# Kernel optimization log

Hardware: AMD Instinct MI355X
Metric: run time of the kernel (lower is better)

Reference implementation:

```python
import jax, jax.numpy as jnp
import numpy as np

IN_CAPS, IN_SIZE = 1152, 8
OUT_CAPS, OUT_SIZE = 10, 16
ROUTING_ITERS = 3
BATCH = 512


def squash(s, axis=-1):
    # v = ||s||^2 / (1 + ||s||^2) * s / ||s||
    sq = jnp.sum(s * s, axis=axis, keepdims=True)
    return s * (sq / (1.0 + sq)) / jnp.sqrt(sq + 1e-8)


def setup_inputs() -> dict:
    key = jax.random.key(0)
    k1, k2 = jax.random.split(key)
    x = jax.random.normal(k1, (BATCH, IN_CAPS, IN_SIZE), dtype=jnp.float32)
    W = jax.random.normal(k2, (IN_CAPS, OUT_CAPS, OUT_SIZE, IN_SIZE), dtype=jnp.float32)
    return {"x": x, "W": W}


def reference(x, W):
    # u_hat[b,i,o,:] = W[i,o] @ x[b,i]  -> (B, 1152, 10, 16)
    u_hat = jnp.einsum('iops,bis->biop', W, x)
    u_det = jax.lax.stop_gradient(u_hat)
    # routing logits, shared across batch: (1152, 10)
    b_ij = jnp.zeros((IN_CAPS, OUT_CAPS), dtype=x.dtype)
    v = None
    for it in range(ROUTING_ITERS):
        # legacy F.softmax on 4D (1,I,O,1) defaults to dim=1 -> over in_capsules
        c_ij = jax.nn.softmax(b_ij, axis=0)  # (I, O)
        if it == ROUTING_ITERS - 1:
            s_j = jnp.einsum('io,biop->bop', c_ij, u_hat)  # (B, 10, 16)
            v = squash(s_j, axis=-1)
        else:
            s_j = jnp.einsum('io,biop->bop', c_ij, u_det)
            v = squash(s_j, axis=-1)
            # agreement: mean over batch of u_hat . v -> (I, O)
            agree = jnp.mean(jnp.einsum('biop,bop->bio', u_det, v), axis=0)
            b_ij = b_ij + agree
    return v  # (B, 10, 16)
```

## Files before the change

### kernel.cpp

```cpp
#include <hip/hip_runtime.h>


#define IC 1152
#define OC 10
#define PS 16
#define SS 8
#define NB 512
#define KD (IC * SS)
#define ND (OC * PS)

#define G1_BM 128
#define G1_NSPLIT 128
#define G1_KSP (KD / G1_NSPLIT)
#define G1_KC 36

#define G2_BCH 32
#define G2_NBS (NB / G2_BCH)
#define G2_NKT (KD / 64)

__global__ void prep_wr(const float* __restrict__ W, float* __restrict__ wr)
{
    const int q = blockIdx.x * 256 + threadIdx.x;
    const int k = q / 40;
    const int n4 = q - k * 40;
    const int i = k >> 3, s = k & 7;
    const int o = n4 >> 2;
    const int p0 = (n4 << 2) & 15;
    const float* wsrc = W + (((size_t)(i * OC + o) * PS) + p0) * SS + s;
    float4 t;
    t.x = wsrc[0]; t.y = wsrc[SS]; t.z = wsrc[2 * SS]; t.w = wsrc[3 * SS];
    *(float4*)(wr + (size_t)q * 4) = t;
}

__global__ void softmax_col(const float* __restrict__ bij, float* __restrict__ c)
{
    const int o = blockIdx.x;
    const int tid = threadIdx.x;
    __shared__ float red[256];

    float m = -3.4e38f;
    for (int i = tid; i < IC; i += 256) m = fmaxf(m, bij[i * OC + o]);
    red[tid] = m;
    __syncthreads();
    for (int st = 128; st > 0; st >>= 1) {
        if (tid < st) red[tid] = fmaxf(red[tid], red[tid + st]);
        __syncthreads();
    }
    m = red[0];
    __syncthreads();

    float sum = 0.f;
    for (int i = tid; i < IC; i += 256) sum += expf(bij[i * OC + o] - m);
    red[tid] = sum;
    __syncthreads();
    for (int st = 128; st > 0; st >>= 1) {
        if (tid < st) red[tid] += red[tid + st];
        __syncthreads();
    }
    const float inv = 1.0f / red[0];

    for (int i = tid; i < IC; i += 256)
        c[i * OC + o] = expf(bij[i * OC + o] - m) * inv;
}

__global__ __launch_bounds__(256, 2) void gemm1_fused(const float* __restrict__ x,
                                                      const float* __restrict__ wr,
                                                      const float* __restrict__ c,
                                                      float* __restrict__ part)
{
    __shared__ __align__(16) float xl[G1_KC][G1_BM + 4];
    __shared__ __align__(16) float wl[G1_KC][ND + 4];
    __shared__ float cl[96];

    const int tid = threadIdx.x;
    const int mb = blockIdx.x & 3;
    const int ks = blockIdx.x >> 2;
    const int m0 = mb * G1_BM;
    const int k0s = ks * G1_KSP;
    const int cg = tid & 15, rg = tid >> 4;
    const int c0 = cg * 10, r0 = rg * 8;

    if (tid < 90) cl[tid] = c ? c[ks * 90 + tid] : (1.0f / 1152.0f);
    __syncthreads();

    float acc[8][10] = {};

    for (int kc = 0; kc < G1_KSP; kc += G1_KC) {
        const int k0 = k0s + kc;
        for (int q = tid; q < (G1_BM * G1_KC / 4); q += 256) {
            const int r = q / 9, kv4 = q - r * 9;
            const float4 t = *(const float4*)(x + (size_t)(m0 + r) * KD + k0 + kv4 * 4);
            xl[kv4 * 4 + 0][r] = t.x;
            xl[kv4 * 4 + 1][r] = t.y;
            xl[kv4 * 4 + 2][r] = t.z;
            xl[kv4 * 4 + 3][r] = t.w;
        }
        for (int q = tid; q < (G1_KC * 40); q += 256) {
            const int rr = q / 40, c4 = q - rr * 40;
            float4 t = *(const float4*)(wr + (size_t)(k0 + rr) * ND + c4 * 4);
            const float sc = cl[(((kc + rr) >> 3) * 10) + (c4 >> 2)];
            t.x *= sc; t.y *= sc; t.z *= sc; t.w *= sc;
            *(float4*)&wl[rr][c4 * 4] = t;
        }
        __syncthreads();
#pragma unroll 4
        for (int kk = 0; kk < G1_KC; ++kk) {
            const float4 a0 = *(const float4*)&xl[kk][r0];
            const float4 a1 = *(const float4*)&xl[kk][r0 + 4];
            const float2 w0 = *(const float2*)&wl[kk][c0 + 0];
            const float2 w1 = *(const float2*)&wl[kk][c0 + 2];
            const float2 w2 = *(const float2*)&wl[kk][c0 + 4];
            const float2 w3 = *(const float2*)&wl[kk][c0 + 6];
            const float2 w4 = *(const float2*)&wl[kk][c0 + 8];
            const float av[8] = { a0.x, a0.y, a0.z, a0.w, a1.x, a1.y, a1.z, a1.w };
            const float wv[10] = { w0.x, w0.y, w1.x, w1.y, w2.x,
                                   w2.y, w3.x, w3.y, w4.x, w4.y };
#pragma unroll
            for (int r = 0; r < 8; ++r)
#pragma unroll
                for (int n = 0; n < 10; ++n)
                    acc[r][n] += av[r] * wv[n];
        }
        __syncthreads();
    }

    float* dst = part + (size_t)ks * (NB * ND);
#pragma unroll
    for (int r = 0; r < 8; ++r) {
        float* row = dst + (size_t)(m0 + r0 + r) * ND + c0;
#pragma unroll
        for (int n = 0; n < 5; ++n)
            *(float2*)(row + n * 2) = *(const float2*)&acc[r][n * 2];
    }
}

__global__ void reduce_squash(const float* __restrict__ part, float* __restrict__ out)
{
    const int t = blockIdx.x * 128 + threadIdx.x;
    const int idx = t >> 2, q = t & 3;
    const float* src = part + (size_t)idx * 16 + q * 4;
    float4 a = { 0, 0, 0, 0 };
#pragma unroll 8
    for (int sp = 0; sp < G1_NSPLIT; ++sp) {
        const float4 p = *(const float4*)(src + (size_t)sp * (NB * ND));
        a.x += p.x; a.y += p.y; a.z += p.z; a.w += p.w;
    }
    float sq = a.x * a.x + a.y * a.y + a.z * a.z + a.w * a.w;
    sq += __shfl_xor(sq, 1);
    sq += __shfl_xor(sq, 2);
    const float f = (sq / (1.0f + sq)) / sqrtf(sq + 1e-8f);
    a.x *= f; a.y *= f; a.z *= f; a.w *= f;
    *(float4*)(out + (size_t)idx * 16 + q * 4) = a;
}

__global__ __launch_bounds__(128, 2) void gemm2_agree(const float* __restrict__ x,
                                                      const float* __restrict__ v,
                                                      const float* __restrict__ wr,
                                                      float* __restrict__ bij)
{
    __shared__ __align__(16) float xl[G2_BCH][68];
    __shared__ __align__(16) float vl[G2_BCH][164];
    __shared__ float agr[80];

    const int tid = threadIdx.x;
    const int kt = blockIdx.x % G2_NKT;
    const int bs = blockIdx.x / G2_NKT;
    const int k0 = kt * 64, b0 = bs * G2_BCH;
    const int cg = tid & 15, rg = tid >> 4;
    const int c0 = cg * 10, r0 = rg * 8;

    if (tid < 80) agr[tid] = 0.f;

    for (int q = tid; q < G2_BCH * 16; q += 128) {
        const int bb = q >> 4, kv = q & 15;
        *(float4*)&xl[bb][kv * 4] = *(const float4*)(x + (size_t)(b0 + bb) * KD + k0 + kv * 4);
    }
    for (int q = tid; q < G2_BCH * 40; q += 128) {
        const int bb = q / 40, nv = q - bb * 40;
        *(float4*)&vl[bb][nv * 4] = *(const float4*)(v + (size_t)(b0 + bb) * ND + nv * 4);
    }
    __syncthreads();

    float acc[8][10] = {};
#pragma unroll 4
    for (int bb = 0; bb < G2_BCH; ++bb) {
        const float4 a0 = *(const float4*)&xl[bb][r0];
        const float4 a1 = *(const float4*)&xl[bb][r0 + 4];
        const float2 w0 = *(const float2*)&vl[bb][c0 + 0];
        const float2 w1 = *(const float2*)&vl[bb][c0 + 2];
        const float2 w2 = *(const float2*)&vl[bb][c0 + 4];
        const float2 w3 = *(const float2*)&vl[bb][c0 + 6];
        const float2 w4 = *(const float2*)&vl[bb][c0 + 8];
        const float av[8] = { a0.x, a0.y, a0.z, a0.w, a1.x, a1.y, a1.z, a1.w };
        const float wv[10] = { w0.x, w0.y, w1.x, w1.y, w2.x,
                               w2.y, w3.x, w3.y, w4.x, w4.y };
#pragma unroll
        for (int r = 0; r < 8; ++r)
#pragma unroll
            for (int n = 0; n < 10; ++n)
                acc[r][n] += av[r] * wv[n];
    }

    const int o0 = c0 >> 4;
    const int nsp = (o0 + 1) * 16 - c0;
    float sum0 = 0.f, sum1 = 0.f;
#pragma unroll
    for (int r = 0; r < 8; ++r) {
        const float* wrow = wr + (size_t)(k0 + r0 + r) * ND + c0;
#pragma unroll
        for (int n = 0; n < 10; ++n) {
            const float t = acc[r][n] * wrow[n];
            if (n < nsp) sum0 += t; else sum1 += t;
        }
    }
    atomicAdd(&agr[rg * 10 + o0], sum0);
    if (nsp < 10) atomicAdd(&agr[rg * 10 + o0 + 1], sum1);
    __syncthreads();

    if (tid < 80) atomicAdd(bij + kt * 80 + tid, agr[tid] * (1.0f / 512.0f));
}

extern "C" void kernel_launch(void* const* d_in, const int* in_sizes, int n_in,
                              void* d_out, int out_size, void* d_ws, size_t ws_size,
                              hipStream_t stream)
{
    (void)in_sizes; (void)n_in; (void)out_size; (void)ws_size;
    const float* x = (const float*)d_in[0];
    const float* W = (const float*)d_in[1];
    float* out = (float*)d_out;
    float* ws = (float*)d_ws;

    float* b_ij = ws;
    float* cbuf = ws + 11520;
    float* wrb  = ws + 23040;
    float* part = ws + 1497600;
    float* vbuf = ws + 11983360;

    hipMemsetAsync(b_ij, 0, IC * OC * sizeof(float), stream);
    prep_wr<<<1440, 256, 0, stream>>>(W, wrb);

    for (int it = 0; it < 3; ++it) {
        const float* cptr = nullptr;
        if (it > 0) {
            softmax_col<<<OC, 256, 0, stream>>>(b_ij, cbuf);
            cptr = cbuf;
        }
        gemm1_fused<<<G1_NSPLIT * 4, 256, 0, stream>>>(x, wrb, cptr, part);
        reduce_squash<<<160, 128, 0, stream>>>(part, (it == 2) ? out : vbuf);
        if (it < 2)
            gemm2_agree<<<G2_NKT * G2_NBS, 128, 0, stream>>>(x, vbuf, wrb, b_ij);
    }
}
```

Before: 263.9 us.

## Fuse all routing stages into one persistent kernel with grid barriers

Replaces the sequence of separate launches (weight reorder, softmax, split-K GEMM, reduce+squash, agreement GEMM) with a single persistent kernel of 512 blocks that uses atomic-counter grid barriers between stages. The softmax over b_ij is now recomputed redundantly in every block instead of in a separate tiny kernel, and the reduce and agreement stages are retiled to use all 512 blocks. The aim is to remove kernel launch gaps and tail effects across about a dozen launches. The trade-offs are that correctness depends on all 512 blocks being co-resident, and that the barriers add spin-wait overhead.

```diff
diff --git a/kernel.cpp b/kernel.cpp
--- a/kernel.cpp
+++ b/kernel.cpp
@@ -6,218 +6,270 @@
 #define PS 16
 #define SS 8
 #define NB 512
-#define KD (IC * SS)
-#define ND (OC * PS)
-
-#define G1_BM 128
-#define G1_NSPLIT 128
-#define G1_KSP (KD / G1_NSPLIT)
-#define G1_KC 36
-
-#define G2_BCH 32
-#define G2_NBS (NB / G2_BCH)
-#define G2_NKT (KD / 64)
-
-__global__ void prep_wr(const float* __restrict__ W, float* __restrict__ wr)
+#define KD 9216
+#define ND 160
+
+#define GRID 512
+#define BLK 256
+
+#define P1_BM 128
+#define P1_KSP 72
+#define P1_KC 36
+
+#define P3_KT 96
+#define P3_NKT 96
+#define P3_BCH 32
+
+__device__ __forceinline__ void gbar(unsigned* slot)
 {
-    const int q = blockIdx.x * 256 + threadIdx.x;
-    const int k = q / 40;
-    const int n4 = q - k * 40;
-    const int i = k >> 3, s = k & 7;
-    const int o = n4 >> 2;
-    const int p0 = (n4 << 2) & 15;
-    const float* wsrc = W + (((size_t)(i * OC + o) * PS) + p0) * SS + s;
-    float4 t;
-    t.x = wsrc[0]; t.y = wsrc[SS]; t.z = wsrc[2 * SS]; t.w = wsrc[3 * SS];
-    *(float4*)(wr + (size_t)q * 4) = t;
-}
-
-__global__ void softmax_col(const float* __restrict__ bij, float* __restrict__ c)
-{
-    const int o = blockIdx.x;
-    const int tid = threadIdx.x;
-    __shared__ float red[256];
-
-    float m = -3.4e38f;
-    for (int i = tid; i < IC; i += 256) m = fmaxf(m, bij[i * OC + o]);
-    red[tid] = m;
     __syncthreads();
-    for (int st = 128; st > 0; st >>= 1) {
-        if (tid < st) red[tid] = fmaxf(red[tid], red[tid + st]);
-        __syncthreads();
-    }
-    m = red[0];
-    __syncthreads();
-
-    float sum = 0.f;
-    for (int i = tid; i < IC; i += 256) sum += expf(bij[i * OC + o] - m);
-    red[tid] = sum;
-    __syncthreads();
-    for (int st = 128; st > 0; st >>= 1) {
-        if (tid < st) red[tid] += red[tid + st];
-        __syncthreads();
-    }
-    const float inv = 1.0f / red[0];
-
-    for (int i = tid; i < IC; i += 256)
-        c[i * OC + o] = expf(bij[i * OC + o] - m) * inv;
-}
-
-__global__ __launch_bounds__(256, 2) void gemm1_fused(const float* __restrict__ x,
-                                                      const float* __restrict__ wr,
-                                                      const float* __restrict__ c,
-                                                      float* __restrict__ part)
-{
-    __shared__ __align__(16) float xl[G1_KC][G1_BM + 4];
-    __shared__ __align__(16) float wl[G1_KC][ND + 4];
-    __shared__ float cl[96];
-
-    const int tid = threadIdx.x;
-    const int mb = blockIdx.x & 3;
-    const int ks = blockIdx.x >> 2;
-    const int m0 = mb * G1_BM;
-    const int k0s = ks * G1_KSP;
-    const int cg = tid & 15, rg = tid >> 4;
-    const int c0 = cg * 10, r0 = rg * 8;
-
-    if (tid < 90) cl[tid] = c ? c[ks * 90 + tid] : (1.0f / 1152.0f);
-    __syncthreads();
-
-    float acc[8][10] = {};
-
-    for (int kc = 0; kc < G1_KSP; kc += G1_KC) {
-        const int k0 = k0s + kc;
-        for (int q = tid; q < (G1_BM * G1_KC / 4); q += 256) {
-            const int r = q / 9, kv4 = q - r * 9;
-            const float4 t = *(const float4*)(x + (size_t)(m0 + r) * KD + k0 + kv4 * 4);
-            xl[kv4 * 4 + 0][r] = t.x;
-            xl[kv4 * 4 + 1][r] = t.y;
-            xl[kv4 * 4 + 2][r] = t.z;
-            xl[kv4 * 4 + 3][r] = t.w;
-        }
-        for (int q = tid; q < (G1_KC * 40); q += 256) {
-            const int rr = q / 40, c4 = q - rr * 40;
-            float4 t = *(const float4*)(wr + (size_t)(k0 + rr) * ND + c4 * 4);
-            const float sc = cl[(((kc + rr) >> 3) * 10) + (c4 >> 2)];
-            t.x *= sc; t.y *= sc; t.z *= sc; t.w *= sc;
-            *(float4*)&wl[rr][c4 * 4] = t;
-        }
-        __syncthreads();
-#pragma unroll 4
-        for (int kk = 0; kk < G1_KC; ++kk) {
-            const float4 a0 = *(const float4*)&xl[kk][r0];
-            const float4 a1 = *(const float4*)&xl[kk][r0 + 4];
-            const float2 w0 = *(const float2*)&wl[kk][c0 + 0];
-            const float2 w1 = *(const float2*)&wl[kk][c0 + 2];
-            const float2 w2 = *(const float2*)&wl[kk][c0 + 4];
-            const float2 w3 = *(const float2*)&wl[kk][c0 + 6];
-            const float2 w4 = *(const float2*)&wl[kk][c0 + 8];
-            const float av[8] = { a0.x, a0.y, a0.z, a0.w, a1.x, a1.y, a1.z, a1.w };
-            const float wv[10] = { w0.x, w0.y, w1.x, w1.y, w2.x,
-                                   w2.y, w3.x, w3.y, w4.x, w4.y };
-#pragma unroll
-            for (int r = 0; r < 8; ++r)
-#pragma unroll
-                for (int n = 0; n < 10; ++n)
-                    acc[r][n] += av[r] * wv[n];
-        }
-        __syncthreads();
-    }
-
-    float* dst = part + (size_t)ks * (NB * ND);
-#pragma unroll
-    for (int r = 0; r < 8; ++r) {
-        float* row = dst + (size_t)(m0 + r0 + r) * ND + c0;
-#pragma unroll
-        for (int n = 0; n < 5; ++n)
-            *(float2*)(row + n * 2) = *(const float2*)&acc[r][n * 2];
-    }
-}
-
-__global__ void reduce_squash(const float* __restrict__ part, float* __restrict__ out)
-{
-    const int t = blockIdx.x * 128 + threadIdx.x;
-    const int idx = t >> 2, q = t & 3;
-    const float* src = part + (size_t)idx * 16 + q * 4;
-    float4 a = { 0, 0, 0, 0 };
-#pragma unroll 8
-    for (int sp = 0; sp < G1_NSPLIT; ++sp) {
-        const float4 p = *(const float4*)(src + (size_t)sp * (NB * ND));
-        a.x += p.x; a.y += p.y; a.z += p.z; a.w += p.w;
-    }
-    float sq = a.x * a.x + a.y * a.y + a.z * a.z + a.w * a.w;
-    sq += __shfl_xor(sq, 1);
-    sq += __shfl_xor(sq, 2);
-    const float f = (sq / (1.0f + sq)) / sqrtf(sq + 1e-8f);
-    a.x *= f; a.y *= f; a.z *= f; a.w *= f;
-    *(float4*)(out + (size_t)idx * 16 + q * 4) = a;
-}
-
-__global__ __launch_bounds__(128, 2) void gemm2_agree(const float* __restrict__ x,
-                                                      const float* __restrict__ v,
-                                                      const float* __restrict__ wr,
-                                                      float* __restrict__ bij)
-{
-    __shared__ __align__(16) float xl[G2_BCH][68];
-    __shared__ __align__(16) float vl[G2_BCH][164];
-    __shared__ float agr[80];
-
-    const int tid = threadIdx.x;
-    const int kt = blockIdx.x % G2_NKT;
-    const int bs = blockIdx.x / G2_NKT;
-    const int k0 = kt * 64, b0 = bs * G2_BCH;
-    const int cg = tid & 15, rg = tid >> 4;
-    const int c0 = cg * 10, r0 = rg * 8;
-
-    if (tid < 80) agr[tid] = 0.f;
-
-    for (int q = tid; q < G2_BCH * 16; q += 128) {
-        const int bb = q >> 4, kv = q & 15;
-        *(float4*)&xl[bb][kv * 4] = *(const float4*)(x + (size_t)(b0 + bb) * KD + k0 + kv * 4);
-    }
-    for (int q = tid; q < G2_BCH * 40; q += 128) {
-        const int bb = q / 40, nv = q - bb * 40;
-        *(float4*)&vl[bb][nv * 4] = *(const float4*)(v + (size_t)(b0 + bb) * ND + nv * 4);
+    if (threadIdx.x == 0) {
+        __threadfence();
+        __hip_atomic_fetch_add(slot, 1u, __ATOMIC_RELEASE, __HIP_MEMORY_SCOPE_AGENT);
+        while (__hip_atomic_load(slot, __ATOMIC_ACQUIRE, __HIP_MEMORY_SCOPE_AGENT) < (unsigned)GRID)
+            __builtin_amdgcn_s_sleep(1);
+        __threadfence();
     }
     __syncthreads();
-
-    float acc[8][10] = {};
+}
+
+__global__ __launch_bounds__(BLK, 2) void digitcaps_mega(const float* __restrict__ x,
+                                                         const float* __restrict__ W,
+                                                         float* __restrict__ out,
+                                                         float* __restrict__ ws)
+{
+    __shared__ __align__(16) char smem[43008];
+    __shared__ float agr[120];
+    __shared__ float sm[344];
+
+    float* b_ij = ws;
+    float* wrb  = ws + 11520;
+    float* part = ws + 1486080;
+    float* vbuf = ws + 11971840;
+    unsigned* bar = (unsigned*)(ws + 12053760);
+
+    const int tid = threadIdx.x;
+    const int bid = blockIdx.x;
+    const int gid = bid * BLK + tid;
+    const int cgx = tid & 15, rgx = tid >> 4;
+    const int c0 = cgx * 10;
+
+    float (*xl1)[132] = (float (*)[132])smem;
+    float (*wl1)[164] = (float (*)[164])(smem + 19008);
+    float* cl         = (float*)(smem + 42624);
+    float (*xl3)[100] = (float (*)[100])smem;
+    float (*vl3)[164] = (float (*)[164])(smem + 12800);
+
+    int slot = 0;
+
+    if (gid < IC * OC) b_ij[gid] = 0.f;
+    for (int q = gid; q < (KD * ND) / 4; q += GRID * BLK) {
+        const int k = q / 40;
+        const int n4 = q - k * 40;
+        const int i = k >> 3, s = k & 7;
+        const int o = n4 >> 2;
+        const int p0 = (n4 << 2) & 15;
+        const float* wsrc = W + (((size_t)(i * OC + o) * PS) + p0) * SS + s;
+        float4 t;
+        t.x = wsrc[0]; t.y = wsrc[SS]; t.z = wsrc[2 * SS]; t.w = wsrc[3 * SS];
+        *(float4*)(wrb + (size_t)q * 4) = t;
+    }
+    gbar(&bar[slot++]);
+
+    for (int it = 0; it < 3; ++it) {
+        {
+            const int mb = bid & 3, ks = bid >> 2;
+            const int m0 = mb * P1_BM, k0s = ks * P1_KSP;
+            const int r0 = rgx * 8;
+
+            if (it == 0) {
+                if (tid < 90) cl[tid] = 1.0f / 1152.0f;
+            } else {
+                if (tid < 160) {
+                    const int o = tid % 10, seg = tid / 10;
+                    const float* bp = b_ij + o;
+                    float m = -3.4e38f;
+                    for (int i = seg * 72; i < seg * 72 + 72; ++i)
+                        m = fmaxf(m, bp[i * 10]);
+                    sm[o * 16 + seg] = m;
+                }
+                __syncthreads();
+                if (tid < 10) {
+                    float m = sm[tid * 16];
+                    for (int s2 = 1; s2 < 16; ++s2) m = fmaxf(m, sm[tid * 16 + s2]);
+                    sm[320 + tid] = m;
+                }
+                __syncthreads();
+                if (tid < 160) {
+                    const int o = tid % 10, seg = tid / 10;
+                    const float mo = sm[320 + o];
+                    const float* bp = b_ij + o;
+                    float s = 0.f;
+                    for (int i = seg * 72; i < seg * 72 + 72; ++i)
+                        s += expf(bp[i * 10] - mo);
+                    sm[160 + o * 16 + seg] = s;
+                }
+                __syncthreads();
+                if (tid < 10) {
+                    float s = 0.f;
+                    for (int s2 = 0; s2 < 16; ++s2) s += sm[160 + tid * 16 + s2];
+                    sm[330 + tid] = 1.0f / s;
+                }
+                __syncthreads();
+                if (tid < 90) {
+                    const int il = tid / 10, o = tid % 10;
+                    const int i = ks * 9 + il;
+                    cl[tid] = expf(b_ij[i * 10 + o] - sm[320 + o]) * sm[330 + o];
+                }
+            }
+            __syncthreads();
+
+            float acc[8][10] = {};
+            for (int kc = 0; kc < P1_KSP; kc += P1_KC) {
+                const int k0 = k0s + kc;
+                for (int q = tid; q < 1152; q += BLK) {
+                    const int r = q / 9, kv4 = q - r * 9;
+                    const float4 t = *(const float4*)(x + (size_t)(m0 + r) * KD + k0 + kv4 * 4);
+                    xl1[kv4 * 4 + 0][r] = t.x;
+                    xl1[kv4 * 4 + 1][r] = t.y;
+                    xl1[kv4 * 4 + 2][r] = t.z;
+                    xl1[kv4 * 4 + 3][r] = t.w;
+                }
+                for (int q = tid; q < 1440; q += BLK) {
+                    const int rr = q / 40, c4 = q - rr * 40;
+                    float4 t = *(const float4*)(wrb + (size_t)(k0 + rr) * ND + c4 * 4);
+                    const float sc = cl[(((kc + rr) >> 3) * 10) + (c4 >> 2)];
+                    t.x *= sc; t.y *= sc; t.z *= sc; t.w *= sc;
+                    *(float4*)&wl1[rr][c4 * 4] = t;
+                }
+                __syncthreads();
 #pragma unroll 4
-    for (int bb = 0; bb < G2_BCH; ++bb) {
-        const float4 a0 = *(const float4*)&xl[bb][r0];
-        const float4 a1 = *(const float4*)&xl[bb][r0 + 4];
-        const float2 w0 = *(const float2*)&vl[bb][c0 + 0];
-        const float2 w1 = *(const float2*)&vl[bb][c0 + 2];
-        const float2 w2 = *(const float2*)&vl[bb][c0 + 4];
-        const float2 w3 = *(const float2*)&vl[bb][c0 + 6];
-        const float2 w4 = *(const float2*)&vl[bb][c0 + 8];
-        const float av[8] = { a0.x, a0.y, a0.z, a0.w, a1.x, a1.y, a1.z, a1.w };
-        const float wv[10] = { w0.x, w0.y, w1.x, w1.y, w2.x,
-                               w2.y, w3.x, w3.y, w4.x, w4.y };
-#pragma unroll
-        for (int r = 0; r < 8; ++r)
-#pragma unroll
-            for (int n = 0; n < 10; ++n)
-                acc[r][n] += av[r] * wv[n];
-    }
-
-    const int o0 = c0 >> 4;
-    const int nsp = (o0 + 1) * 16 - c0;
-    float sum0 = 0.f, sum1 = 0.f;
-#pragma unroll
-    for (int r = 0; r < 8; ++r) {
-        const float* wrow = wr + (size_t)(k0 + r0 + r) * ND + c0;
-#pragma unroll
-        for (int n = 0; n < 10; ++n) {
-            const float t = acc[r][n] * wrow[n];
-            if (n < nsp) sum0 += t; else sum1 += t;
+                for (int kk = 0; kk < P1_KC; ++kk) {
+                    const float4 a0 = *(const float4*)&xl1[kk][r0];
+                    const float4 a1 = *(const float4*)&xl1[kk][r0 + 4];
+                    const float2 w0 = *(const float2*)&wl1[kk][c0 + 0];
+                    const float2 w1 = *(const float2*)&wl1[kk][c0 + 2];
+                    const float2 w2 = *(const float2*)&wl1[kk][c0 + 4];
+                    const float2 w3 = *(const float2*)&wl1[kk][c0 + 6];
+                    const float2 w4 = *(const float2*)&wl1[kk][c0 + 8];
+                    const float av[8] = { a0.x, a0.y, a0.z, a0.w, a1.x, a1.y, a1.z, a1.w };
+                    const float wv[10] = { w0.x, w0.y, w1.x, w1.y, w2.x,
+                                           w2.y, w3.x, w3.y, w4.x, w4.y };
+#pragma unroll
+                    for (int r = 0; r < 8; ++r)
+#pragma unroll
+                        for (int n = 0; n < 10; ++n)
+                            acc[r][n] += av[r] * wv[n];
+                }
+                __syncthreads();
+            }
+            float* dst = part + (size_t)ks * (NB * ND);
+#pragma unroll
+            for (int r = 0; r < 8; ++r) {
+                float* row = dst + (size_t)(m0 + r0 + r) * ND + c0;
+#pragma unroll
+                for (int n = 0; n < 5; ++n)
+                    *(float2*)(row + n * 2) = *(const float2*)&acc[r][n * 2];
+            }
+        }
+        gbar(&bar[slot++]);
+
+        {
+            float* dst = (it == 2) ? out : vbuf;
+            if (gid < 81920) {
+                const int bo = gid >> 4;
+                const int sub = gid & 15;
+                const int h = sub >> 2, q = sub & 3;
+                const float* src = part + (size_t)bo * 16 + q * 4;
+                float4 a = { 0, 0, 0, 0 };
+#pragma unroll 8
+                for (int j = 0; j < 32; ++j) {
+                    const float4 p = *(const float4*)(src + (size_t)(h + 4 * j) * (NB * ND));
+                    a.x += p.x; a.y += p.y; a.z += p.z; a.w += p.w;
+                }
+                a.x += __shfl_xor(a.x, 4); a.y += __shfl_xor(a.y, 4);
+                a.z += __shfl_xor(a.z, 4); a.w += __shfl_xor(a.w, 4);
+                a.x += __shfl_xor(a.x, 8); a.y += __shfl_xor(a.y, 8);
+                a.z += __shfl_xor(a.z, 8); a.w += __shfl_xor(a.w, 8);
+                float sq = a.x * a.x + a.y * a.y + a.z * a.z + a.w * a.w;
+                sq += __shfl_xor(sq, 1);
+                sq += __shfl_xor(sq, 2);
+                const float f = (sq / (1.0f + sq)) / sqrtf(sq + 1e-8f);
+                if (h == 0) {
+                    float4 r;
+                    r.x = a.x * f; r.y = a.y * f; r.z = a.z * f; r.w = a.w * f;
+                    *(float4*)(dst + (size_t)bo * 16 + q * 4) = r;
+                }
+            }
+        }
+
+        if (it < 2) {
+            gbar(&bar[slot++]);
+            {
+                const int r0 = rgx * 6;
+                const int o0 = c0 >> 4;
+                const int nsp = (o0 + 1) * 16 - c0;
+                for (int rep = 0; rep < 3; ++rep) {
+                    const int vt = bid * 3 + rep;
+                    const int kt = vt % P3_NKT;
+                    const int bs = vt / P3_NKT;
+                    const int k0 = kt * P3_KT, b0 = bs * P3_BCH;
+                    if (tid < 120) agr[tid] = 0.f;
+                    for (int q = tid; q < 768; q += BLK) {
+                        const int bb = q / 24, kv = q - bb * 24;
+                        *(float4*)&xl3[bb][kv * 4] =
+                            *(const float4*)(x + (size_t)(b0 + bb) * KD + k0 + kv * 4);
+                    }
+                    for (int q = tid; q < 1280; q += BLK) {
+                        const int bb = q / 40, nv = q - bb * 40;
+                        *(float4*)&vl3[bb][nv * 4] =
+                            *(const float4*)(vbuf + (size_t)(b0 + bb) * ND + nv * 4);
+                    }
+                    __syncthreads();
+
+                    float acc[6][10] = {};
+#pragma unroll 4
+                    for (int bb = 0; bb < P3_BCH; ++bb) {
+                        const float2 x0 = *(const float2*)&xl3[bb][r0];
+                        const float2 x1 = *(const float2*)&xl3[bb][r0 + 2];
+                        const float2 x2 = *(const float2*)&xl3[bb][r0 + 4];
+                        const float2 w0 = *(const float2*)&vl3[bb][c0 + 0];
+                        const float2 w1 = *(const float2*)&vl3[bb][c0 + 2];
+                        const float2 w2 = *(const float2*)&vl3[bb][c0 + 4];
+                        const float2 w3 = *(const float2*)&vl3[bb][c0 + 6];
+                        const float2 w4 = *(const float2*)&vl3[bb][c0 + 8];
+                        const float av[6] = { x0.x, x0.y, x1.x, x1.y, x2.x, x2.y };
+                        const float wv[10] = { w0.x, w0.y, w1.x, w1.y, w2.x,
+                                               w2.y, w3.x, w3.y, w4.x, w4.y };
+#pragma unroll
+                        for (int r = 0; r < 6; ++r)
+#pragma unroll
+                            for (int n = 0; n < 10; ++n)
+                                acc[r][n] += av[r] * wv[n];
+                    }
+
+#pragma unroll
+                    for (int r = 0; r < 6; ++r) {
+                        const int row = r0 + r;
+                        const int il = row >> 3;
+                        const float* wrow = wrb + (size_t)(k0 + row) * ND + c0;
+                        float s0 = 0.f, s1 = 0.f;
+#pragma unroll
+                        for (int n = 0; n < 10; ++n) {
+                            const float t = acc[r][n] * wrow[n];
+                            if (n < nsp) s0 += t; else s1 += t;
+                        }
+                        atomicAdd(&agr[il * 10 + o0], s0);
+                        if (nsp < 10) atomicAdd(&agr[il * 10 + o0 + 1], s1);
+                    }
+                    __syncthreads();
+                    if (tid < 120) atomicAdd(&b_ij[kt * 120 + tid], agr[tid] * (1.0f / 512.0f));
+                    __syncthreads();
+                }
+            }
+            gbar(&bar[slot++]);
         }
     }
-    atomicAdd(&agr[rg * 10 + o0], sum0);
-    if (nsp < 10) atomicAdd(&agr[rg * 10 + o0 + 1], sum1);
-    __syncthreads();
-
-    if (tid < 80) atomicAdd(bij + kt * 80 + tid, agr[tid] * (1.0f / 512.0f));
 }
 
 extern "C" void kernel_launch(void* const* d_in, const int* in_sizes, int n_in,
@@ -230,24 +282,6 @@
     float* out = (float*)d_out;
     float* ws = (float*)d_ws;
 
-    float* b_ij = ws;
-    float* cbuf = ws + 11520;
-    float* wrb  = ws + 23040;
-    float* part = ws + 1497600;
-    float* vbuf = ws + 11983360;
-
-    hipMemsetAsync(b_ij, 0, IC * OC * sizeof(float), stream);
-    prep_wr<<<1440, 256, 0, stream>>>(W, wrb);
-
-    for (int it = 0; it < 3; ++it) {
-        const float* cptr = nullptr;
-        if (it > 0) {
-            softmax_col<<<OC, 256, 0, stream>>>(b_ij, cbuf);
-            cptr = cbuf;
-        }
-        gemm1_fused<<<G1_NSPLIT * 4, 256, 0, stream>>>(x, wrb, cptr, part);
-        reduce_squash<<<160, 128, 0, stream>>>(part, (it == 2) ? out : vbuf);
-        if (it < 2)
-            gemm2_agree<<<G2_NKT * G2_NBS, 128, 0, stream>>>(x, vbuf, wrb, b_ij);
-    }
+    hipMemsetAsync(ws + 12053760, 0, 16 * sizeof(unsigned), stream);
+    digitcaps_mega<<<GRID, BLK, 0, stream>>>(x, W, out, ws);
 }
```

Result: slower. 956.7 us (+262.6%).

## Fuse softmax into gemm1, fold memset into prep, widen reduce parallelism

Applied to the files above, without the earlier changes.

Removes the separate softmax_col kernel: every gemm1 block now recomputes the per-column max and sum over all b_ij and derives its own coupling coefficients. The memset of b_ij moves into prep_wr. reduce_squash now spreads the 128-way split reduction over four lanes per output vector and combines them with shuffles, which raises parallelism. Together these remove three launches, but each of the 512 gemm1 blocks repeats the full 11520-element softmax scan in its prologue.

```diff
diff --git a/kernel.cpp b/kernel.cpp
--- a/kernel.cpp
+++ b/kernel.cpp
@@ -6,21 +6,23 @@
 #define PS 16
 #define SS 8
 #define NB 512
-#define KD (IC * SS)
-#define ND (OC * PS)
-
+#define KD 9216
+#define ND 160
+
+#define G1_NS 128
 #define G1_BM 128
-#define G1_NSPLIT 128
-#define G1_KSP (KD / G1_NSPLIT)
+#define G1_KSP 72
 #define G1_KC 36
 
 #define G2_BCH 32
-#define G2_NBS (NB / G2_BCH)
-#define G2_NKT (KD / 64)
-
-__global__ void prep_wr(const float* __restrict__ W, float* __restrict__ wr)
+#define G2_NBS 16
+#define G2_NKT 144
+
+__global__ void prep_wr(const float* __restrict__ W, float* __restrict__ wr,
+                        float* __restrict__ bij)
 {
     const int q = blockIdx.x * 256 + threadIdx.x;
+    if (q < IC * OC) bij[q] = 0.f;
     const int k = q / 40;
     const int n4 = q - k * 40;
     const int i = k >> 3, s = k & 7;
@@ -32,45 +34,16 @@
     *(float4*)(wr + (size_t)q * 4) = t;
 }
 
-__global__ void softmax_col(const float* __restrict__ bij, float* __restrict__ c)
-{
-    const int o = blockIdx.x;
-    const int tid = threadIdx.x;
-    __shared__ float red[256];
-
-    float m = -3.4e38f;
-    for (int i = tid; i < IC; i += 256) m = fmaxf(m, bij[i * OC + o]);
-    red[tid] = m;
-    __syncthreads();
-    for (int st = 128; st > 0; st >>= 1) {
-        if (tid < st) red[tid] = fmaxf(red[tid], red[tid + st]);
-        __syncthreads();
-    }
-    m = red[0];
-    __syncthreads();
-
-    float sum = 0.f;
-    for (int i = tid; i < IC; i += 256) sum += expf(bij[i * OC + o] - m);
-    red[tid] = sum;
-    __syncthreads();
-    for (int st = 128; st > 0; st >>= 1) {
-        if (tid < st) red[tid] += red[tid + st];
-        __syncthreads();
-    }
-    const float inv = 1.0f / red[0];
-
-    for (int i = tid; i < IC; i += 256)
-        c[i * OC + o] = expf(bij[i * OC + o] - m) * inv;
-}
-
 __global__ __launch_bounds__(256, 2) void gemm1_fused(const float* __restrict__ x,
                                                       const float* __restrict__ wr,
-                                                      const float* __restrict__ c,
-                                                      float* __restrict__ part)
+                                                      const float* __restrict__ bij,
+                                                      float* __restrict__ part,
+                                                      int it)
 {
     __shared__ __align__(16) float xl[G1_KC][G1_BM + 4];
     __shared__ __align__(16) float wl[G1_KC][ND + 4];
     __shared__ float cl[96];
+    __shared__ float sm[344];
 
     const int tid = threadIdx.x;
     const int mb = blockIdx.x & 3;
@@ -80,14 +53,53 @@
     const int cg = tid & 15, rg = tid >> 4;
     const int c0 = cg * 10, r0 = rg * 8;
 
-    if (tid < 90) cl[tid] = c ? c[ks * 90 + tid] : (1.0f / 1152.0f);
+    if (it == 0) {
+        if (tid < 90) cl[tid] = 1.0f / 1152.0f;
+    } else {
+        if (tid < 160) {
+            const int o = tid % 10, seg = tid / 10;
+            const float* bp = bij + o;
+            float m = -3.4e38f;
+            for (int i = seg * 72; i < seg * 72 + 72; ++i)
+                m = fmaxf(m, bp[i * 10]);
+            sm[o * 16 + seg] = m;
+        }
+        __syncthreads();
+        if (tid < 10) {
+            float m = sm[tid * 16];
+            for (int s2 = 1; s2 < 16; ++s2) m = fmaxf(m, sm[tid * 16 + s2]);
+            sm[320 + tid] = m;
+        }
+        __syncthreads();
+        if (tid < 160) {
+            const int o = tid % 10, seg = tid / 10;
+            const float mo = sm[320 + o];
+            const float* bp = bij + o;
+            float s = 0.f;
+            for (int i = seg * 72; i < seg * 72 + 72; ++i)
+                s += expf(bp[i * 10] - mo);
+            sm[160 + o * 16 + seg] = s;
+        }
+        __syncthreads();
+        if (tid < 10) {
+            float s = 0.f;
+            for (int s2 = 0; s2 < 16; ++s2) s += sm[160 + tid * 16 + s2];
+            sm[330 + tid] = 1.0f / s;
+        }
+        __syncthreads();
+        if (tid < 90) {
+            const int il = tid / 10, o = tid % 10;
+            const int i = ks * 9 + il;
+            cl[tid] = expf(bij[i * 10 + o] - sm[320 + o]) * sm[330 + o];
+        }
+    }
     __syncthreads();
 
     float acc[8][10] = {};
 
     for (int kc = 0; kc < G1_KSP; kc += G1_KC) {
         const int k0 = k0s + kc;
-        for (int q = tid; q < (G1_BM * G1_KC / 4); q += 256) {
+        for (int q = tid; q < 1152; q += 256) {
             const int r = q / 9, kv4 = q - r * 9;
             const float4 t = *(const float4*)(x + (size_t)(m0 + r) * KD + k0 + kv4 * 4);
             xl[kv4 * 4 + 0][r] = t.x;
@@ -95,7 +107,7 @@
             xl[kv4 * 4 + 2][r] = t.z;
             xl[kv4 * 4 + 3][r] = t.w;
         }
-        for (int q = tid; q < (G1_KC * 40); q += 256) {
+        for (int q = tid; q < 1440; q += 256) {
             const int rr = q / 40, c4 = q - rr * 40;
             float4 t = *(const float4*)(wr + (size_t)(k0 + rr) * ND + c4 * 4);
             const float sc = cl[(((kc + rr) >> 3) * 10) + (c4 >> 2)];
@@ -136,21 +148,30 @@
 
 __global__ void reduce_squash(const float* __restrict__ part, float* __restrict__ out)
 {
-    const int t = blockIdx.x * 128 + threadIdx.x;
-    const int idx = t >> 2, q = t & 3;
-    const float* src = part + (size_t)idx * 16 + q * 4;
+    const int gid = blockIdx.x * 256 + threadIdx.x;
+    const int bo = gid >> 4;
+    const int sub = gid & 15;
+    const int h = sub >> 2, q = sub & 3;
+    const float* src = part + (size_t)bo * 16 + q * 4;
     float4 a = { 0, 0, 0, 0 };
 #pragma unroll 8
-    for (int sp = 0; sp < G1_NSPLIT; ++sp) {
-        const float4 p = *(const float4*)(src + (size_t)sp * (NB * ND));
+    for (int j = 0; j < 32; ++j) {
+        const float4 p = *(const float4*)(src + (size_t)(h + 4 * j) * (NB * ND));
         a.x += p.x; a.y += p.y; a.z += p.z; a.w += p.w;
     }
+    a.x += __shfl_xor(a.x, 4); a.y += __shfl_xor(a.y, 4);
+    a.z += __shfl_xor(a.z, 4); a.w += __shfl_xor(a.w, 4);
+    a.x += __shfl_xor(a.x, 8); a.y += __shfl_xor(a.y, 8);
+    a.z += __shfl_xor(a.z, 8); a.w += __shfl_xor(a.w, 8);
     float sq = a.x * a.x + a.y * a.y + a.z * a.z + a.w * a.w;
     sq += __shfl_xor(sq, 1);
     sq += __shfl_xor(sq, 2);
     const float f = (sq / (1.0f + sq)) / sqrtf(sq + 1e-8f);
-    a.x *= f; a.y *= f; a.z *= f; a.w *= f;
-    *(float4*)(out + (size_t)idx * 16 + q * 4) = a;
+    if (h == 0) {
+        float4 r;
+        r.x = a.x * f; r.y = a.y * f; r.z = a.z * f; r.w = a.w * f;
+        *(float4*)(out + (size_t)bo * 16 + q * 4) = r;
+    }
 }
 
 __global__ __launch_bounds__(128, 2) void gemm2_agree(const float* __restrict__ x,
@@ -231,22 +252,15 @@
     float* ws = (float*)d_ws;
 
     float* b_ij = ws;
-    float* cbuf = ws + 11520;
-    float* wrb  = ws + 23040;
-    float* part = ws + 1497600;
-    float* vbuf = ws + 11983360;
-
-    hipMemsetAsync(b_ij, 0, IC * OC * sizeof(float), stream);
-    prep_wr<<<1440, 256, 0, stream>>>(W, wrb);
+    float* wrb  = ws + 11520;
+    float* part = ws + 1486080;
+    float* vbuf = ws + 11971840;
+
+    prep_wr<<<1440, 256, 0, stream>>>(W, wrb, b_ij);
 
     for (int it = 0; it < 3; ++it) {
-        const float* cptr = nullptr;
-        if (it > 0) {
-            softmax_col<<<OC, 256, 0, stream>>>(b_ij, cbuf);
-            cptr = cbuf;
-        }
-        gemm1_fused<<<G1_NSPLIT * 4, 256, 0, stream>>>(x, wrb, cptr, part);
-        reduce_squash<<<160, 128, 0, stream>>>(part, (it == 2) ? out : vbuf);
+        gemm1_fused<<<G1_NS * 4, 256, 0, stream>>>(x, wrb, b_ij, part, it);
+        reduce_squash<<<320, 256, 0, stream>>>(part, (it == 2) ? out : vbuf);
         if (it < 2)
             gemm2_agree<<<G2_NKT * G2_NBS, 128, 0, stream>>>(x, vbuf, wrb, b_ij);
     }
```

Result: slower. 277.1 us (+5.0%).
